# Kernel optimization log

Measured on AMD Instinct MI355X. Metric: run time of the kernel, lower is better.

Reference implementation:

```python
import jax, jax.numpy as jnp
import numpy as np

B, S, E, H = 8, 2048, 512, 8
D = E // H  # head_dim = 64


def setup_inputs() -> dict:
    key0 = jax.random.key(0)
    ks = jax.random.split(key0, 12)
    scale = 1.0 / np.sqrt(E)
    return {
        "value": jax.random.normal(ks[0], (B, S, E), jnp.float32),
        "key": jax.random.normal(ks[1], (B, S, E), jnp.float32),
        "query": jax.random.normal(ks[2], (B, S, E), jnp.float32),
        "mask": jax.random.randint(ks[3], (B, 1, 1, S), 0, 2, jnp.int32),
        "wq": jax.random.normal(ks[4], (E, E), jnp.float32) * scale,
        "bq": jnp.zeros((E,), jnp.float32),
        "wk": jax.random.normal(ks[5], (E, E), jnp.float32) * scale,
        "bk": jnp.zeros((E,), jnp.float32),
        "wv": jax.random.normal(ks[6], (E, E), jnp.float32) * scale,
        "bv": jnp.zeros((E,), jnp.float32),
        "wo": jax.random.normal(ks[7], (E, E), jnp.float32) * scale,
        "bo": jnp.zeros((E,), jnp.float32),
    }


def reference(value, key, query, mask, wq, bq, wk, bk, wv, bv, wo, bo):
    b, s, e = query.shape
    # projections
    q = (query @ wq + bq).reshape(b, s, H, D)  # (B,S,H,D)
    k = (key @ wk + bk).reshape(b, s, H, D)
    v = (value @ wv + bv).reshape(b, s, H, D)
    # scaled dot-product logits: (B,H,Sq,Sk)
    logits = jnp.einsum("bqhd,bkhd->bhqk", q, k) / jnp.sqrt(jnp.asarray(D, q.dtype))
    logits = logits + mask.astype(logits.dtype) * -1e9  # mask==1 -> blocked
    attn = jax.nn.softmax(logits, axis=-1)
    out = jnp.einsum("bhqk,bkhd->bqhd", attn, v).reshape(b, s, e)
    return out @ wo + bo
```

## Files before the change

### kernel.cpp

```cpp
#include <hip/hip_runtime.h>

#define Bz 8
#define Sz 2048
#define Ez 512
#define Hz 8
#define Dz 64

typedef _Float16 f16;
typedef __attribute__((ext_vector_type(2))) _Float16 f16x2;
typedef __attribute__((ext_vector_type(8))) _Float16 f16x8;
typedef __attribute__((ext_vector_type(4))) float f32x4;

#define LOG2E 1.44269504f

__device__ __forceinline__ void async16(const void* g, void* l) {
    __builtin_amdgcn_global_load_lds(
        (const __attribute__((address_space(1))) unsigned int*)g,
        (__attribute__((address_space(3))) unsigned int*)l, 16, 0, 0);
}

__device__ __forceinline__ f16x2 pkrtz(float a, float b) {
    return __builtin_bit_cast(f16x2, __builtin_amdgcn_cvt_pkrtz(a, b));
}

__device__ __forceinline__ int swz(int row) {
    return (row & 7) ^ ((2 * ((row >> 3) & 3)) & 7);
}

__global__ __launch_bounds__(256)
void cast_kernel(const float* __restrict__ q, const float* __restrict__ k,
                 const float* __restrict__ v, const int* __restrict__ mask,
                 f16* __restrict__ qa, f16* __restrict__ ka, f16* __restrict__ va,
                 int* __restrict__ rnk, int* __restrict__ slen, f16* __restrict__ vt)
{
    const int z = blockIdx.y;
    const int tid = threadIdx.x;
    if (z == 3) {
        const int b = blockIdx.x;
        if (b >= Bz) return;
        __shared__ int sc2[2][256];
        __shared__ int ssl;
        const int* mp = mask + (size_t)b * Sz;
        int m[8], c = 0;
        #pragma unroll
        for (int j = 0; j < 8; ++j) { m[j] = mp[tid*8 + j]; c += (m[j] == 0); }
        sc2[0][tid] = c;
        __syncthreads();
        int src = 0;
        #pragma unroll
        for (int s = 1; s < 256; s <<= 1) {
            int vv = sc2[src][tid] + ((tid >= s) ? sc2[src][tid - s] : 0);
            sc2[src ^ 1][tid] = vv;
            src ^= 1;
            __syncthreads();
        }
        int incl = sc2[src][tid];
        int base = incl - c;
        if (tid == 255) { slen[b] = incl; ssl = incl; }
        int kk = base;
        int r8[8];
        #pragma unroll
        for (int j = 0; j < 8; ++j) {
            r8[j] = (m[j] == 0) ? kk : -1;
            kk += (m[j] == 0);
        }
        #pragma unroll
        for (int j = 0; j < 8; ++j) rnk[(size_t)b * Sz + tid*8 + j] = r8[j];
        __syncthreads();
        const int sl2 = ssl;
        const int pad = (sl2 + 63) & ~63;
        if (pad > sl2) {
            for (int pr = tid; pr < Hz * Dz; pr += 256) {
                f16* dst = vt + ((size_t)b * Hz * Dz + pr) * Sz;
                for (int j = sl2; j < pad; ++j) dst[j] = (f16)0.f;
            }
        }
        return;
    }
    const int i = blockIdx.x * 256 + tid;
    const float* src = (z == 0) ? q : (z == 1) ? k : v;
    f16* dst = (z == 0) ? qa : (z == 1) ? ka : va;
    float4 x = *(const float4*)&src[(size_t)i * 4];
    f16x2 h0 = pkrtz(x.x, x.y), h1 = pkrtz(x.z, x.w);
    f16 h[4] = {h0[0], h0[1], h1[0], h1[1]};
    *(uint2*)&dst[(size_t)i * 4] = *(uint2*)h;
}

__global__ __launch_bounds__(256)
void prep_w(const float* __restrict__ W0, const float* __restrict__ W1,
            const float* __restrict__ W2, const float* __restrict__ W3,
            f16* __restrict__ T0, f16* __restrict__ T1,
            f16* __restrict__ T2, f16* __restrict__ T3)
{
    __shared__ float S[64][68];
    const float* W = (blockIdx.z==0)?W0:(blockIdx.z==1)?W1:(blockIdx.z==2)?W2:W3;
    f16*         T = (blockIdx.z==0)?T0:(blockIdx.z==1)?T1:(blockIdx.z==2)?T2:T3;
    const float sc = (blockIdx.z == 0) ? 0.125f * LOG2E : 1.0f;
    const int k0 = blockIdx.x * 64, n0 = blockIdx.y * 64;
    const int tid = threadIdx.x;
    {
        int kr = tid >> 4, nc = (tid & 15) * 4;
        #pragma unroll
        for (int i = 0; i < 4; ++i) {
            float4 w4 = *(const float4*)&W[(size_t)(k0 + kr + i*16) * Ez + n0 + nc];
            S[kr + i*16][nc+0] = w4.x; S[kr + i*16][nc+1] = w4.y;
            S[kr + i*16][nc+2] = w4.z; S[kr + i*16][nc+3] = w4.w;
        }
    }
    __syncthreads();
    {
        int n = tid >> 2, kq = tid & 3;
        f16 h[16];
        #pragma unroll
        for (int j = 0; j < 16; ++j) h[j] = (f16)(S[kq*16 + j][n] * sc);
        f16* dst = &T[(size_t)(n0 + n) * Ez + k0 + kq*16];
        *(uint4*)&dst[0] = *(uint4*)&h[0];
        *(uint4*)&dst[8] = *(uint4*)&h[8];
    }
}

__global__ __launch_bounds__(256, 4)
void proj_gemm(const f16* __restrict__ qa, const f16* __restrict__ ka,
               const f16* __restrict__ va,
               const f16* __restrict__ wtq, const f16* __restrict__ wtk,
               const f16* __restrict__ wtv,
               const float* __restrict__ bqp, const float* __restrict__ bkp,
               const float* __restrict__ bvp, const int* __restrict__ rnk,
               f16* __restrict__ qp, f16* __restrict__ kp, f16* __restrict__ vt)
{
    __shared__ __align__(16) char lds[32768];
    const int z = blockIdx.z;
    const f16* A  = (z==0)?qa:(z==1)?ka:va;
    const f16* Wt = (z==0)?wtq:(z==1)?wtk:wtv;
    const float* bias = (z==0)?bqp:(z==1)?bkp:bvp;
    const float bscale = (z==0) ? 0.125f*LOG2E : 1.0f;

    const int tid  = threadIdx.x;
    const int lane = tid & 63, w = tid >> 6;
    const int col  = lane & 15, quad = lane >> 4;
    const int wm = w & 1, wn = w >> 1;
    const int m0 = blockIdx.x * 128, n0 = blockIdx.y * 128;
    const int srow = lane >> 2, schunk = lane & 3;

    f32x4 acc[4][4];
    #pragma unroll
    for (int i = 0; i < 4; ++i)
        #pragma unroll
        for (int j = 0; j < 4; ++j) acc[i][j] = (f32x4){0.f,0.f,0.f,0.f};

    auto issue = [&](int t, int buf) {
        f16* As = (f16*)(lds + buf * 16384);
        f16* Ws = As + 4096;
        #pragma unroll
        for (int i = 0; i < 2; ++i) {
            int row = w*32 + i*16 + srow;
            int cl = schunk ^ ((row >> 1) & 3);
            async16(&A[(size_t)(m0 + row) * Ez + t*32 + cl*8],  &As[row*32 + schunk*8]);
            async16(&Wt[(size_t)(n0 + row) * Ez + t*32 + cl*8], &Ws[row*32 + schunk*8]);
        }
    };

    issue(0, 0);
    const int xrc = (col >> 1) & 3;

    for (int t = 0; t < 16; ++t) {
        const int cur = t & 1;
        __syncthreads();
        if (t < 15) issue(t + 1, cur ^ 1);
        f16* As = (f16*)(lds + cur * 16384);
        f16* Ws = As + 4096;
        f16x8 af[4];
        #pragma unroll
        for (int mi = 0; mi < 4; ++mi)
            af[mi] = *(const f16x8*)&As[(wm*64 + mi*16 + col)*32 + ((quad ^ xrc)*8)];
        #pragma unroll
        for (int ni = 0; ni < 4; ++ni) {
            f16x8 wf = *(const f16x8*)&Ws[(wn*64 + ni*16 + col)*32 + ((quad ^ xrc)*8)];
            #pragma unroll
            for (int mi = 0; mi < 4; ++mi)
                acc[mi][ni] = __builtin_amdgcn_mfma_f32_16x16x32_f16(af[mi], wf, acc[mi][ni], 0,0,0);
        }
    }

    const int bb = m0 >> 11;
    const int TS = (z == 2) ? 73 : 72;

    int* rks  = (int*)(lds + 20480);
    int* clp  = (int*)(lds + 22528);
    int* sr0p = (int*)(lds + 24576);
    int r0v = 0x7fffffff;
    if (z == 2) {
        __syncthreads();
        if (tid == 0) sr0p[0] = 0x7fffffff;
        if (tid < 128) clp[tid] = -1;
        __syncthreads();
        if (tid < 128) {
            int rb = rnk[(size_t)bb * Sz + ((m0 + tid) & (Sz - 1))];
            rks[tid] = rb;
            if (rb >= 0) atomicMin(sr0p, rb);
        }
        __syncthreads();
        r0v = sr0p[0];
        if (tid < 128) {
            int rb = rks[tid];
            if (rb >= 0) clp[rb - r0v] = tid;
        }
    }

    const int rw = tid >> 1, half = tid & 1;
    const int s = (m0 + rw) & (Sz - 1);
    int rowout = s;
    bool dostore = true;
    if (z == 1) {
        int rk = rnk[(size_t)bb * Sz + s];
        dostore = (rk >= 0);
        rowout = rk;
    }

    f16* Tr = (f16*)lds;
    #pragma unroll
    for (int p = 0; p < 2; ++p) {
        __syncthreads();
        if (wn == p) {
            #pragma unroll
            for (int ni = 0; ni < 4; ++ni) {
                float bv = bias[n0 + p*64 + ni*16 + col] * bscale;
                #pragma unroll
                for (int mi = 0; mi < 4; ++mi)
                    #pragma unroll
                    for (int rr = 0; rr < 4; ++rr) {
                        int ml = wm*64 + mi*16 + quad*4 + rr;
                        Tr[ml*TS + ni*16 + col] = (f16)(acc[mi][ni][rr] + bv);
                    }
            }
        }
        __syncthreads();
        const int hh = (n0 >> 6) + p;
        if (z != 2) {
            if (dostore) {
                f16* C16 = (z == 0) ? qp : kp;
                f16* dst = &C16[(((size_t)bb*Hz + hh)*Sz + rowout)*Dz + half*32];
                const f16* srcp = &Tr[rw*TS + half*32];
                #pragma unroll
                for (int j = 0; j < 4; ++j)
                    *(uint4*)&dst[j*8] = *(const uint4*)&srcp[j*8];
            }
        } else if (r0v != 0x7fffffff) {
            const int jlane = tid & 63, dgrp = tid >> 6;
            #pragma unroll
            for (int dd = 0; dd < 16; ++dd) {
                const int d = dgrp * 16 + dd;
                f16* dstb = vt + (((size_t)bb * Hz + hh) * Dz + d) * Sz + r0v;
                #pragma unroll
                for (int jh = 0; jh < 2; ++jh) {
                    const int j = jh * 64 + jlane;
                    const int sr = clp[j];
                    if (sr >= 0) dstb[j] = Tr[sr * 73 + d];
                }
            }
        }
    }
}

__global__ __launch_bounds__(256, 4)
void out_gemm(const f16* __restrict__ A, const f16* __restrict__ Wt,
              const float* __restrict__ bias, float* __restrict__ Cf)
{
    __shared__ __align__(16) char lds[32768];
    const int tid  = threadIdx.x;
    const int lane = tid & 63, w = tid >> 6;
    const int col  = lane & 15, quad = lane >> 4;
    const int wm = w & 1, wn = w >> 1;
    const int m0 = blockIdx.x * 128, n0 = blockIdx.y * 128;
    const int srow = lane >> 2, schunk = lane & 3;

    f32x4 acc[4][4];
    #pragma unroll
    for (int i = 0; i < 4; ++i)
        #pragma unroll
        for (int j = 0; j < 4; ++j) acc[i][j] = (f32x4){0.f,0.f,0.f,0.f};

    auto issue = [&](int t, int buf) {
        f16* As = (f16*)(lds + buf * 16384);
        f16* Ws = As + 4096;
        #pragma unroll
        for (int i = 0; i < 2; ++i) {
            int row = w*32 + i*16 + srow;
            int cl = schunk ^ ((row >> 1) & 3);
            async16(&A[(size_t)(m0 + row) * Ez + t*32 + cl*8],  &As[row*32 + schunk*8]);
            async16(&Wt[(size_t)(n0 + row) * Ez + t*32 + cl*8], &Ws[row*32 + schunk*8]);
        }
    };

    issue(0, 0);
    const int xrc = (col >> 1) & 3;

    for (int t = 0; t < 16; ++t) {
        const int cur = t & 1;
        __syncthreads();
        if (t < 15) issue(t + 1, cur ^ 1);
        f16* As = (f16*)(lds + cur * 16384);
        f16* Ws = As + 4096;
        f16x8 af[4];
        #pragma unroll
        for (int mi = 0; mi < 4; ++mi)
            af[mi] = *(const f16x8*)&As[(wm*64 + mi*16 + col)*32 + ((quad ^ xrc)*8)];
        #pragma unroll
        for (int ni = 0; ni < 4; ++ni) {
            f16x8 wf = *(const f16x8*)&Ws[(wn*64 + ni*16 + col)*32 + ((quad ^ xrc)*8)];
            #pragma unroll
            for (int mi = 0; mi < 4; ++mi)
                acc[mi][ni] = __builtin_amdgcn_mfma_f32_16x16x32_f16(af[mi], wf, acc[mi][ni], 0,0,0);
        }
    }

    #pragma unroll
    for (int ni = 0; ni < 4; ++ni) {
        int n = n0 + wn*64 + ni*16 + col;
        float bv = bias[n];
        #pragma unroll
        for (int mi = 0; mi < 4; ++mi)
            #pragma unroll
            for (int rr = 0; rr < 4; ++rr) {
                int m = m0 + wm*64 + mi*16 + quad*4 + rr;
                Cf[(size_t)m * Ez + n] = acc[mi][ni][rr] + bv;
            }
    }
}

__global__ __launch_bounds__(256, 4)
void attn_f16(const f16* __restrict__ Q, const f16* __restrict__ K,
              const f16* __restrict__ VT, const int* __restrict__ slen,
              f16* __restrict__ O)
{
    __shared__ __align__(16) f16 KS[2][64*64];
    __shared__ __align__(16) f16 VS[2][64*64];

    const int tid  = threadIdx.x;
    const int lane = tid & 63, w = tid >> 6;
    const int col  = lane & 15, quad = lane >> 4;

    const int blk = blockIdx.x;
    const int xcd = blk & 7, slot = blk >> 3;
    const int bh = xcd + 8 * (slot >> 4);
    const int qb = slot & 15;
    const int b = bh >> 3, h = bh & 7;

    const int sl = slen[b];
    int nt = (sl + 63) >> 6;
    if (nt < 1) nt = 1;

    const int q0 = qb * 128 + w * 32;

    f16x8 qf[2][2];
    #pragma unroll
    for (int qt = 0; qt < 2; ++qt)
        #pragma unroll
        for (int ks = 0; ks < 2; ++ks)
            qf[qt][ks] = *(const f16x8*)&Q[((size_t)bh*Sz + q0 + qt*16 + col)*Dz + ks*32 + quad*8];

    const f16* Kp = K + (size_t)bh * Sz * Dz;
    const f16* Vp = VT + (size_t)bh * Dz * Sz;

    const int srow = lane >> 3, sch = lane & 7;
    const int row0 = w*16 + srow, row1 = row0 + 8;
    const int cl0 = sch ^ swz(row0), cl1 = sch ^ swz(row1);

    int keyrow[4], gk[4];
    #pragma unroll
    for (int kc = 0; kc < 4; ++kc) {
        keyrow[kc] = 32*(kc>>1) + 8*(col>>2) + 4*(kc&1) + (col&3);
        gk[kc] = swz(keyrow[kc]);
    }

    f32x4 oacc[2][4];
    #pragma unroll
    for (int qt = 0; qt < 2; ++qt)
        #pragma unroll
        for (int dc = 0; dc < 4; ++dc) oacc[qt][dc] = (f32x4){0.f,0.f,0.f,0.f};
    const f32x4 zero4 = (f32x4){0.f, 0.f, 0.f, 0.f};
    f32x4 lacc[2] = {(f32x4){0.f,0.f,0.f,0.f}, (f32x4){0.f,0.f,0.f,0.f}};
    f16x8 one8;
    #pragma unroll
    for (int i = 0; i < 8; ++i) one8[i] = (f16)1.0f;

    auto issue = [&](int t, int buf) {
        async16(&Kp[(size_t)(t*64 + row0)*Dz + cl0*8], &KS[buf][row0*64 + sch*8]);
        async16(&Vp[(size_t)row0*Sz + t*64 + cl0*8],   &VS[buf][row0*64 + sch*8]);
        async16(&Kp[(size_t)(t*64 + row1)*Dz + cl1*8], &KS[buf][row1*64 + sch*8]);
        async16(&Vp[(size_t)row1*Sz + t*64 + cl1*8],   &VS[buf][row1*64 + sch*8]);
    };

    issue(0, 0);

    for (int t = 0; t < nt; ++t) {
        const int cur = t & 1;
        __syncthreads();
        if (t + 1 < nt) issue(t + 1, cur ^ 1);

        f32x4 sc[2][4];
        __builtin_amdgcn_s_setprio(1);
        #pragma unroll
        for (int kc = 0; kc < 4; ++kc) {
            f16x8 kf0 = *(const f16x8*)&KS[cur][keyrow[kc]*64 + ((quad ^ gk[kc])*8)];
            f16x8 kf1 = *(const f16x8*)&KS[cur][keyrow[kc]*64 + (((4 + quad) ^ gk[kc])*8)];
            sc[0][kc] = __builtin_amdgcn_mfma_f32_16x16x32_f16(kf0, qf[0][0], zero4, 0,0,0);
            sc[1][kc] = __builtin_amdgcn_mfma_f32_16x16x32_f16(kf0, qf[1][0], zero4, 0,0,0);
            sc[0][kc] = __builtin_amdgcn_mfma_f32_16x16x32_f16(kf1, qf[0][1], sc[0][kc], 0,0,0);
            sc[1][kc] = __builtin_amdgcn_mfma_f32_16x16x32_f16(kf1, qf[1][1], sc[1][kc], 0,0,0);
        }
        __builtin_amdgcn_s_setprio(0);

        const bool last = (t == nt - 1);
        union { f16x2 h2[4]; f16x8 h8; } ph[2][2];
        #pragma unroll
        for (int qt = 0; qt < 2; ++qt) {
            #pragma unroll
            for (int kg = 0; kg < 2; ++kg) {
                float e0 = __builtin_amdgcn_exp2f(sc[qt][2*kg][0]);
                float e1 = __builtin_amdgcn_exp2f(sc[qt][2*kg][1]);
                float e2 = __builtin_amdgcn_exp2f(sc[qt][2*kg][2]);
                float e3 = __builtin_amdgcn_exp2f(sc[qt][2*kg][3]);
                float e4 = __builtin_amdgcn_exp2f(sc[qt][2*kg+1][0]);
                float e5 = __builtin_amdgcn_exp2f(sc[qt][2*kg+1][1]);
                float e6 = __builtin_amdgcn_exp2f(sc[qt][2*kg+1][2]);
                float e7 = __builtin_amdgcn_exp2f(sc[qt][2*kg+1][3]);
                if (last) {
                    int rem = sl - t*64 - 32*kg - 8*quad;
                    e0 = (rem > 0) ? e0 : 0.f; e1 = (rem > 1) ? e1 : 0.f;
                    e2 = (rem > 2) ? e2 : 0.f; e3 = (rem > 3) ? e3 : 0.f;
                    e4 = (rem > 4) ? e4 : 0.f; e5 = (rem > 5) ? e5 : 0.f;
                    e6 = (rem > 6) ? e6 : 0.f; e7 = (rem > 7) ? e7 : 0.f;
                }
                ph[qt][kg].h2[0] = pkrtz(e0, e1);
                ph[qt][kg].h2[1] = pkrtz(e2, e3);
                ph[qt][kg].h2[2] = pkrtz(e4, e5);
                ph[qt][kg].h2[3] = pkrtz(e6, e7);
            }
        }

        __builtin_amdgcn_s_setprio(1);
        lacc[0] = __builtin_amdgcn_mfma_f32_16x16x32_f16(one8, ph[0][0].h8, lacc[0], 0,0,0);
        lacc[1] = __builtin_amdgcn_mfma_f32_16x16x32_f16(one8, ph[1][0].h8, lacc[1], 0,0,0);
        lacc[0] = __builtin_amdgcn_mfma_f32_16x16x32_f16(one8, ph[0][1].h8, lacc[0], 0,0,0);
        lacc[1] = __builtin_amdgcn_mfma_f32_16x16x32_f16(one8, ph[1][1].h8, lacc[1], 0,0,0);
        #pragma unroll
        for (int dc = 0; dc < 4; ++dc) {
            const int d = dc*16 + col;
            const int gd = swz(d);
            #pragma unroll
            for (int kg = 0; kg < 2; ++kg) {
                f16x8 vf = *(const f16x8*)&VS[cur][d*64 + (((kg*4 + quad) ^ gd)*8)];
                oacc[0][dc] = __builtin_amdgcn_mfma_f32_16x16x32_f16(vf, ph[0][kg].h8, oacc[0][dc], 0,0,0);
                oacc[1][dc] = __builtin_amdgcn_mfma_f32_16x16x32_f16(vf, ph[1][kg].h8, oacc[1][dc], 0,0,0);
            }
        }
        __builtin_amdgcn_s_setprio(0);
    }

    float inv[2];
    inv[0] = 1.0f / lacc[0][0];
    inv[1] = 1.0f / lacc[1][0];
    #pragma unroll
    for (int qt = 0; qt < 2; ++qt) {
        const int q = q0 + qt*16 + col;
        f16* op = &O[((size_t)b*Sz + q)*Ez + h*Dz];
        #pragma unroll
        for (int dc = 0; dc < 4; ++dc) {
            f16 ov[4] = {(f16)(oacc[qt][dc][0]*inv[qt]), (f16)(oacc[qt][dc][1]*inv[qt]),
                         (f16)(oacc[qt][dc][2]*inv[qt]), (f16)(oacc[qt][dc][3]*inv[qt])};
            *(uint2*)&op[dc*16 + quad*4] = *(uint2*)ov;
        }
    }
}

extern "C" void kernel_launch(void* const* d_in, const int* in_sizes, int n_in,
                              void* d_out, int out_size, void* d_ws, size_t ws_size,
                              hipStream_t stream)
{
    const float* value = (const float*)d_in[0];
    const float* key   = (const float*)d_in[1];
    const float* query = (const float*)d_in[2];
    const int*   mask  = (const int*)d_in[3];
    const float* wq = (const float*)d_in[4];
    const float* bq = (const float*)d_in[5];
    const float* wk = (const float*)d_in[6];
    const float* bk = (const float*)d_in[7];
    const float* wv = (const float*)d_in[8];
    const float* bv = (const float*)d_in[9];
    const float* wo = (const float*)d_in[10];
    const float* bo = (const float*)d_in[11];
    float* out = (float*)d_out;

    const size_t nW   = (size_t)Ez * Ez;
    const size_t nAct = (size_t)Bz * Sz * Ez;
    f16* wtq = (f16*)d_ws;
    f16* wtk = wtq + nW;
    f16* wtv = wtk + nW;
    f16* wto = wtv + nW;
    f16* qa  = wto + nW;
    f16* ka  = qa + nAct;
    f16* va  = ka + nAct;
    f16* qp  = va + nAct;
    f16* kp  = qp + nAct;
    f16* vt  = kp + nAct;
    f16* o16 = vt + nAct;
    int* rnkp = (int*)(o16 + nAct);
    int* slenp = rnkp + Bz * Sz;

    cast_kernel<<<dim3(8192, 4), 256, 0, stream>>>(query, key, value, mask,
                                                   qa, ka, va, rnkp, slenp, vt);
    prep_w<<<dim3(8, 8, 4), 256, 0, stream>>>(wq, wk, wv, wo, wtq, wtk, wtv, wto);

    proj_gemm<<<dim3(128, 4, 3), 256, 0, stream>>>(qa, ka, va, wtq, wtk, wtv,
                                                   bq, bk, bv, rnkp, qp, kp, vt);

    attn_f16<<<1024, 256, 0, stream>>>(qp, kp, vt, slenp, o16);

    out_gemm<<<dim3(128, 4), 256, 0, stream>>>(o16, wto, bo, out);
}
```

Before: 278.0 us.

## Gather unmasked key/value rows before projection and skip fully masked tiles

The mask scan now writes a compacted index list of unmasked positions instead of per-position ranks. The K and V projection GEMMs gather their input rows through that list, so each tile computes only rows that survive the mask, and blocks past the unmasked length return early, roughly halving K/V projection work. The V transpose store becomes a contiguous vectorized write through a transposed LDS tile, replacing scattered per-element stores. This adds an index load per row and clamped duplicate rows in the last partial tile.

```diff
diff --git a/kernel.cpp b/kernel.cpp
--- a/kernel.cpp
+++ b/kernel.cpp
@@ -31,7 +31,7 @@
 void cast_kernel(const float* __restrict__ q, const float* __restrict__ k,
                  const float* __restrict__ v, const int* __restrict__ mask,
                  f16* __restrict__ qa, f16* __restrict__ ka, f16* __restrict__ va,
-                 int* __restrict__ rnk, int* __restrict__ slen, f16* __restrict__ vt)
+                 int* __restrict__ idx, int* __restrict__ slen, f16* __restrict__ vt)
 {
     const int z = blockIdx.y;
     const int tid = threadIdx.x;
@@ -58,14 +58,9 @@
         int base = incl - c;
         if (tid == 255) { slen[b] = incl; ssl = incl; }
         int kk = base;
-        int r8[8];
-        #pragma unroll
-        for (int j = 0; j < 8; ++j) {
-            r8[j] = (m[j] == 0) ? kk : -1;
-            kk += (m[j] == 0);
-        }
-        #pragma unroll
-        for (int j = 0; j < 8; ++j) rnk[(size_t)b * Sz + tid*8 + j] = r8[j];
+        #pragma unroll
+        for (int j = 0; j < 8; ++j)
+            if (m[j] == 0) idx[(size_t)b * Sz + (kk++)] = tid*8 + j;
         __syncthreads();
         const int sl2 = ssl;
         const int pad = (sl2 + 63) & ~63;
@@ -125,11 +120,22 @@
                const f16* __restrict__ wtq, const f16* __restrict__ wtk,
                const f16* __restrict__ wtv,
                const float* __restrict__ bqp, const float* __restrict__ bkp,
-               const float* __restrict__ bvp, const int* __restrict__ rnk,
+               const float* __restrict__ bvp, const int* __restrict__ idx,
+               const int* __restrict__ slen,
                f16* __restrict__ qp, f16* __restrict__ kp, f16* __restrict__ vt)
 {
     __shared__ __align__(16) char lds[32768];
     const int z = blockIdx.z;
+    const int m0 = blockIdx.x * 128, n0 = blockIdx.y * 128;
+    const int bb = m0 >> 11;
+    const int m0c = m0 & (Sz - 1);
+
+    int sl = Sz;
+    if (z != 0) {
+        sl = slen[bb];
+        if (m0c >= sl) return;
+    }
+
     const f16* A  = (z==0)?qa:(z==1)?ka:va;
     const f16* Wt = (z==0)?wtq:(z==1)?wtk:wtv;
     const float* bias = (z==0)?bqp:(z==1)?bkp:bvp;
@@ -139,8 +145,24 @@
     const int lane = tid & 63, w = tid >> 6;
     const int col  = lane & 15, quad = lane >> 4;
     const int wm = w & 1, wn = w >> 1;
-    const int m0 = blockIdx.x * 128, n0 = blockIdx.y * 128;
     const int srow = lane >> 2, schunk = lane & 3;
+
+    size_t rb[2];
+    int clv[2];
+    #pragma unroll
+    for (int i = 0; i < 2; ++i) {
+        const int row = w*32 + i*16 + srow;
+        clv[i] = schunk ^ ((row >> 1) & 3);
+        const int j = m0c + row;
+        int srcrow;
+        if (z == 0) {
+            srcrow = j;
+        } else {
+            const int jc = (j < sl) ? j : sl - 1;
+            srcrow = idx[(size_t)bb * Sz + jc];
+        }
+        rb[i] = ((size_t)bb * Sz + srcrow) * Ez;
+    }
 
     f32x4 acc[4][4];
     #pragma unroll
@@ -153,10 +175,9 @@
         f16* Ws = As + 4096;
         #pragma unroll
         for (int i = 0; i < 2; ++i) {
-            int row = w*32 + i*16 + srow;
-            int cl = schunk ^ ((row >> 1) & 3);
-            async16(&A[(size_t)(m0 + row) * Ez + t*32 + cl*8],  &As[row*32 + schunk*8]);
-            async16(&Wt[(size_t)(n0 + row) * Ez + t*32 + cl*8], &Ws[row*32 + schunk*8]);
+            const int row = w*32 + i*16 + srow;
+            async16(&A[rb[i] + t*32 + clv[i]*8],                    &As[row*32 + schunk*8]);
+            async16(&Wt[(size_t)(n0 + row) * Ez + t*32 + clv[i]*8], &Ws[row*32 + schunk*8]);
         }
     };
 
@@ -182,42 +203,10 @@
         }
     }
 
-    const int bb = m0 >> 11;
-    const int TS = (z == 2) ? 73 : 72;
-
-    int* rks  = (int*)(lds + 20480);
-    int* clp  = (int*)(lds + 22528);
-    int* sr0p = (int*)(lds + 24576);
-    int r0v = 0x7fffffff;
-    if (z == 2) {
-        __syncthreads();
-        if (tid == 0) sr0p[0] = 0x7fffffff;
-        if (tid < 128) clp[tid] = -1;
-        __syncthreads();
-        if (tid < 128) {
-            int rb = rnk[(size_t)bb * Sz + ((m0 + tid) & (Sz - 1))];
-            rks[tid] = rb;
-            if (rb >= 0) atomicMin(sr0p, rb);
-        }
-        __syncthreads();
-        r0v = sr0p[0];
-        if (tid < 128) {
-            int rb = rks[tid];
-            if (rb >= 0) clp[rb - r0v] = tid;
-        }
-    }
-
     const int rw = tid >> 1, half = tid & 1;
-    const int s = (m0 + rw) & (Sz - 1);
-    int rowout = s;
-    bool dostore = true;
-    if (z == 1) {
-        int rk = rnk[(size_t)bb * Sz + s];
-        dostore = (rk >= 0);
-        rowout = rk;
-    }
-
-    f16* Tr = (f16*)lds;
+
+    f16* Tr  = (f16*)lds;
+    f16* Tr2 = (f16*)lds;
     #pragma unroll
     for (int p = 0; p < 2; ++p) {
         __syncthreads();
@@ -229,33 +218,41 @@
                 for (int mi = 0; mi < 4; ++mi)
                     #pragma unroll
                     for (int rr = 0; rr < 4; ++rr) {
-                        int ml = wm*64 + mi*16 + quad*4 + rr;
-                        Tr[ml*TS + ni*16 + col] = (f16)(acc[mi][ni][rr] + bv);
+                        const int ml = wm*64 + mi*16 + quad*4 + rr;
+                        const float val = acc[mi][ni][rr] + bv;
+                        if (z != 2) Tr[ml*72 + ni*16 + col] = (f16)val;
+                        else        Tr2[(ni*16 + col)*136 + ml] = (f16)val;
                     }
             }
         }
         __syncthreads();
         const int hh = (n0 >> 6) + p;
         if (z != 2) {
-            if (dostore) {
+            const int rank = m0c + rw;
+            if (z == 0 || rank < sl) {
                 f16* C16 = (z == 0) ? qp : kp;
-                f16* dst = &C16[(((size_t)bb*Hz + hh)*Sz + rowout)*Dz + half*32];
-                const f16* srcp = &Tr[rw*TS + half*32];
+                f16* dst = &C16[(((size_t)bb*Hz + hh)*Sz + rank)*Dz + half*32];
+                const f16* srcp = &Tr[rw*72 + half*32];
                 #pragma unroll
                 for (int j = 0; j < 4; ++j)
                     *(uint4*)&dst[j*8] = *(const uint4*)&srcp[j*8];
             }
-        } else if (r0v != 0x7fffffff) {
-            const int jlane = tid & 63, dgrp = tid >> 6;
-            #pragma unroll
-            for (int dd = 0; dd < 16; ++dd) {
-                const int d = dgrp * 16 + dd;
-                f16* dstb = vt + (((size_t)bb * Hz + hh) * Dz + d) * Sz + r0v;
-                #pragma unroll
-                for (int jh = 0; jh < 2; ++jh) {
-                    const int j = jh * 64 + jlane;
-                    const int sr = clp[j];
-                    if (sr >= 0) dstb[j] = Tr[sr * 73 + d];
+        } else {
+            const int d = tid >> 2, mq = tid & 3;
+            const int base = m0c + mq*32;
+            if (base < sl) {
+                f16* dstb = vt + (((size_t)bb*Hz + hh)*Dz + d)*Sz + base;
+                const f16* srcr = &Tr2[d*136 + mq*32];
+                int lim = sl - base; if (lim > 32) lim = 32;
+                if (lim == 32) {
+                    #pragma unroll
+                    for (int g = 0; g < 4; ++g)
+                        *(uint4*)&dstb[g*8] = *(const uint4*)&srcr[g*8];
+                } else {
+                    const int full = lim >> 3;
+                    for (int g = 0; g < full; ++g)
+                        *(uint4*)&dstb[g*8] = *(const uint4*)&srcr[g*8];
+                    for (int e = full*8; e < lim; ++e) dstb[e] = srcr[e];
                 }
             }
         }
@@ -505,15 +502,16 @@
     f16* kp  = qp + nAct;
     f16* vt  = kp + nAct;
     f16* o16 = vt + nAct;
-    int* rnkp = (int*)(o16 + nAct);
-    int* slenp = rnkp + Bz * Sz;
+    int* idxp = (int*)(o16 + nAct);
+    int* slenp = idxp + Bz * Sz;
 
     cast_kernel<<<dim3(8192, 4), 256, 0, stream>>>(query, key, value, mask,
-                                                   qa, ka, va, rnkp, slenp, vt);
+                                                   qa, ka, va, idxp, slenp, vt);
     prep_w<<<dim3(8, 8, 4), 256, 0, stream>>>(wq, wk, wv, wo, wtq, wtk, wtv, wto);
 
     proj_gemm<<<dim3(128, 4, 3), 256, 0, stream>>>(qa, ka, va, wtq, wtk, wtv,
-                                                   bq, bk, bv, rnkp, qp, kp, vt);
+                                                   bq, bk, bv, idxp, slenp,
+                                                   qp, kp, vt);
 
     attn_f16<<<1024, 256, 0, stream>>>(qp, kp, vt, slenp, o16);
 
```

New measurement: 272.1 us. -2.1%, faster.
